# Kernel optimization log

Hardware: AMD Instinct MI355X
Metric: run time of the kernel (lower is better)

The kernel has to match this reference:

```python
import jax, jax.numpy as jnp
import numpy as np

B, N_NOISY, N_CLEAN = 4, 4096, 4500
N_TRAIN = 128          # num_train_points
FRAME_KNN = 32         # K
NUM_CLEAN_NBS = 4      # C
DSM_SIGMA = 0.01
FEAT_KNN = 16          # knn inside feature extractor
FE_HID, FEAT_DIM = 64, 128
HID = 128              # score_net_hidden_dim
NUM_BLOCKS = 4
C_DIM = FEAT_DIM + 3   # z_dim + xyz dim


def _sqdist(a, b):
    # a: (..., n, d), b: (..., m, d) -> (..., n, m)
    return (jnp.sum(a * a, -1)[..., :, None]
            + jnp.sum(b * b, -1)[..., None, :]
            - 2.0 * jnp.einsum('...nd,...md->...nm', a, b))


def _knn_idx(q, ref, k):
    _, idx = jax.lax.top_k(-_sqdist(q, ref), k)
    return idx


def _feature_net(pcl, W1, b1, W2, b2):
    # EdgeConv-style point feature extractor: knn gather -> MLP -> max-reduce
    Bb = pcl.shape[0]
    idx = _knn_idx(pcl, pcl, FEAT_KNN)                       # (B,N,k)
    nbrs = pcl[jnp.arange(Bb)[:, None, None], idx]           # (B,N,k,3)
    ctr = pcl[:, :, None, :]
    edge = jnp.concatenate([jnp.broadcast_to(ctr, nbrs.shape), nbrs - ctr], -1)
    h = jnp.max(jax.nn.relu(edge @ W1 + b1), axis=2)         # (B,N,FE_HID)
    return jax.nn.relu(h @ W2 + b2)                          # (B,N,FEAT_DIM)


def _bn(x, g, b):
    # eval-mode BatchNorm1d with default running stats (mean=0, var=1): affine only
    return x * g + b


def _score_net(x, c, Wp, bp, g0, b0, W0, bf0, g1, b1, W1, bf1, Wc, bc, gO, bO, Wo, bo):
    # x: (M,K,3) centered neighbor frames, c: (M,F) per-point latent -> (M,K,1)
    M, K, _ = x.shape
    c_xyz = jnp.concatenate([x, jnp.broadcast_to(c[:, None, :], (M, K, c.shape[-1]))], -1)
    net = c_xyz @ Wp + bp
    for i in range(NUM_BLOCKS):  # ResnetBlockConv1d, conditioned on c_xyz
        h = jax.nn.relu(_bn(net, g0[i], b0[i])) @ W0[i] + bf0[i]
        dx = jax.nn.relu(_bn(h, g1[i], b1[i])) @ W1[i] + bf1[i]
        net = net + dx + c_xyz @ Wc[i] + bc[i]
    return jax.nn.relu(_bn(net, gO, bO)) @ Wo + bo


def setup_inputs() -> dict:
    key = jax.random.key(0)
    ks = jax.random.split(key, 16)
    s = 0.05
    inp = {
        'pcl_noisy': jax.random.normal(ks[0], (B, N_NOISY, 3), jnp.float32),
        'pcl_clean': jax.random.normal(ks[1], (B, N_CLEAN, 3), jnp.float32),
        'pnt_idx': jax.random.randint(ks[2], (N_TRAIN,), 0, N_NOISY),
        # feature net
        'feW1': s * jax.random.normal(ks[3], (6, FE_HID), jnp.float32),
        'feb1': jnp.zeros((FE_HID,), jnp.float32),
        'feW2': s * jax.random.normal(ks[4], (FE_HID, FEAT_DIM), jnp.float32),
        'feb2': jnp.zeros((FEAT_DIM,), jnp.float32),
        # score net
        'Wp': s * jax.random.normal(ks[5], (C_DIM, HID), jnp.float32),
        'bp': jnp.zeros((HID,), jnp.float32),
        'g0': jnp.ones((NUM_BLOCKS, HID), jnp.float32),
        'b0': jnp.zeros((NUM_BLOCKS, HID), jnp.float32),
        'W0': s * jax.random.normal(ks[6], (NUM_BLOCKS, HID, HID), jnp.float32),
        'bf0': jnp.zeros((NUM_BLOCKS, HID), jnp.float32),
        'g1': jnp.ones((NUM_BLOCKS, HID), jnp.float32),
        'b1': jnp.zeros((NUM_BLOCKS, HID), jnp.float32),
        'W1': s * jax.random.normal(ks[7], (NUM_BLOCKS, HID, HID), jnp.float32),
        'bf1': jnp.zeros((NUM_BLOCKS, HID), jnp.float32),
        'Wc': s * jax.random.normal(ks[8], (NUM_BLOCKS, C_DIM, HID), jnp.float32),
        'bc': jnp.zeros((NUM_BLOCKS, HID), jnp.float32),
        'gO': jnp.ones((HID,), jnp.float32),
        'bO': jnp.zeros((HID,), jnp.float32),
        'Wo': s * jax.random.normal(ks[9], (HID, 1), jnp.float32),
        'bo': jnp.zeros((1,), jnp.float32),
    }
    return inp


def reference(pcl_noisy, pcl_clean, pnt_idx, feW1, feb1, feW2, feb2,
              Wp, bp, g0, b0, W0, bf0, g1, b1, W1, bf1, Wc, bc, gO, bO, Wo, bo):
    Bb, N, _ = pcl_noisy.shape
    n, K, C = pnt_idx.shape[0], FRAME_KNN, NUM_CLEAN_NBS
    bidx = jnp.arange(Bb)[:, None]
    # per-point features at training points
    feat = _feature_net(pcl_noisy, feW1, feb1, feW2, feb2)[:, pnt_idx]  # (B,n,F)
    centers = pcl_noisy[:, pnt_idx]                                     # (B,n,3)
    # xy-KNN over noisy cloud -> gather 3D neighbor frames, center them
    nn_idx = _knn_idx(centers[..., :2], pcl_noisy[..., :2], K)           # (B,n,K)
    frames = pcl_noisy[bidx, nn_idx.reshape(Bb, -1)].reshape(Bb, n, K, 3)
    frames_centered = frames - centers[:, :, None, :]
    # xy-KNN of each frame point into the clean cloud
    cidx = _knn_idx(frames[..., :2].reshape(Bb, n * K, 2), pcl_clean[..., :2], C)
    clean_nbs = pcl_clean[bidx, cidx.reshape(Bb, -1)].reshape(Bb, n, K, C, 3)
    # z-only noise vectors, mean over clean neighbors
    noise_z = jnp.mean(frames[..., 2][..., None] - clean_nbs[..., 2], axis=-1)[..., None]  # (B,n,K,1)
    grad_pred = _score_net(frames_centered.reshape(Bb * n, K, 3), feat.reshape(Bb * n, -1),
                           Wp, bp, g0, b0, W0, bf0, g1, b1, W1, bf1, Wc, bc,
                           gO, bO, Wo, bo).reshape(Bb, n, K, 1)
    grad_target = -noise_z
    loss = 0.5 * jnp.mean(jnp.sum((grad_target - grad_pred) ** 2 * (1.0 / DSM_SIGMA), axis=-1))
    return loss
```

## Files before the change

### kernel.cpp

```cpp
#include <hip/hip_runtime.h>
#include <stdint.h>

#define NB_B 4
#define NN 4096
#define NC 4500
#define NT 128
#define FRAME_K 32
#define FEAT_K 16
#define FE_HID 64
#define FEAT_DIM 128
#define HID 128
#define HIDP (HID + 4)
#define NUM_BLOCKS 4

typedef unsigned long long ull;
typedef __attribute__((ext_vector_type(8))) short bf16x8;
typedef __attribute__((ext_vector_type(4))) float f32x4;

__device__ __forceinline__ ull pack_di(float d, int i) {
    return (((ull)__float_as_uint(d)) << 32) | (uint32_t)(unsigned)i;
}

__device__ __forceinline__ unsigned short f2bf(float f) {
    uint32_t u = __float_as_uint(f);
    return (unsigned short)((u + 0x7fffu + ((u >> 16) & 1u)) >> 16);
}

#define UMIN(a,b) ((a) < (b) ? (a) : (b))

#define INS4(v) do { ull _v=(v); if (_v < t3) { if (_v < t2) { t3=t2; \
    if (_v < t1) { t2=t1; if (_v < t0) { t1=t0; t0=_v; } else t1=_v; } \
    else t2=_v; } else t3=_v; } } while(0)

#define LMIN16(dst, v) do { \
    ull _a0 = UMIN(v[0], v[1]),  _a1 = UMIN(v[2], v[3]); \
    ull _a2 = UMIN(v[4], v[5]),  _a3 = UMIN(v[6], v[7]); \
    ull _a4 = UMIN(v[8], v[9]),  _a5 = UMIN(v[10], v[11]); \
    ull _a6 = UMIN(v[12], v[13]),_a7 = UMIN(v[14], v[15]); \
    ull _b0 = UMIN(_a0, _a1), _b1 = UMIN(_a2, _a3); \
    ull _b2 = UMIN(_a4, _a5), _b3 = UMIN(_a6, _a7); \
    dst = UMIN(UMIN(_b0, _b1), UMIN(_b2, _b3)); \
} while(0)

__global__ __launch_bounds__(256) void k_prep(
    const float* __restrict__ W0, const float* __restrict__ W1,
    unsigned short* __restrict__ W0T, unsigned short* __restrict__ W1T)
{
    int idx = blockIdx.x * 256 + threadIdx.x;
    int k = idx & 127, n = (idx >> 7) & 127, blk = idx >> 14;
    int src = blk * 16384 + k * 128 + n;
    W0T[idx] = f2bf(W0[src]);
    W1T[idx] = f2bf(W1[src]);
}

__global__ __launch_bounds__(256) void k_nbr(
    const float* __restrict__ pcl, const int* __restrict__ pidx,
    const float* __restrict__ W1, const float* __restrict__ b1,
    const float* __restrict__ W2, const float* __restrict__ b2,
    float* __restrict__ feat_out,
    float* __restrict__ frames, float* __restrict__ framesC)
{
    int blk = blockIdx.x;
    int b = blk >> 7;
    int i = blk & 127;
    int t = threadIdx.x;
    int wave = t >> 6, lane = t & 63;
    __shared__ ull wred[2][4];
    __shared__ float nb[FEAT_K][3];
    __shared__ float hmax[FE_HID];
    const float* P = pcl + b * NN * 3;
    int qi = pidx[i];
    float qx = P[qi*3+0], qy = P[qi*3+1], qz = P[qi*3+2];

    ull v3[16], v2[16];
    #pragma unroll
    for (int c2 = 0; c2 < 16; ++c2) {
        int j = t + c2*256;
        float dx = P[j*3+0]-qx, dy = P[j*3+1]-qy, dz = P[j*3+2]-qz;
        float dd2 = dx*dx + dy*dy;
        v2[c2] = pack_di(dd2, j);
        v3[c2] = pack_di(dd2 + dz*dz, j);
    }

    int mysel3 = 0, mysel2 = 0;

    {
        ull mymin;
        LMIN16(mymin, v3);
        for (int r = 0; r < FEAT_K; ++r) {
            ull wm = mymin;
            for (int mask = 1; mask < 64; mask <<= 1) {
                ull o = __shfl_xor(wm, mask, 64);
                wm = UMIN(wm, o);
            }
            if (lane == 0) wred[r & 1][wave] = wm;
            __syncthreads();
            ull w0 = wred[r&1][0], w1 = wred[r&1][1];
            ull w2 = wred[r&1][2], w3 = wred[r&1][3];
            ull ww = UMIN(UMIN(w0, w1), UMIN(w2, w3));
            if (t == r) mysel3 = (int)(ww & 0xffffffffu);
            if (mymin == ww) {
                #pragma unroll
                for (int c2 = 0; c2 < 16; ++c2)
                    if (v3[c2] == ww) v3[c2] = ~0ull;
                LMIN16(mymin, v3);
            }
        }
    }
    {
        ull mymin;
        LMIN16(mymin, v2);
        for (int r = 0; r < FRAME_K; ++r) {
            ull wm = mymin;
            for (int mask = 1; mask < 64; mask <<= 1) {
                ull o = __shfl_xor(wm, mask, 64);
                wm = UMIN(wm, o);
            }
            if (lane == 0) wred[r & 1][wave] = wm;
            __syncthreads();
            ull w0 = wred[r&1][0], w1 = wred[r&1][1];
            ull w2 = wred[r&1][2], w3 = wred[r&1][3];
            ull ww = UMIN(UMIN(w0, w1), UMIN(w2, w3));
            if (t == r) mysel2 = (int)(ww & 0xffffffffu);
            if (mymin == ww) {
                #pragma unroll
                for (int c2 = 0; c2 < 16; ++c2)
                    if (v2[c2] == ww) v2[c2] = ~0ull;
                LMIN16(mymin, v2);
            }
        }
    }

    if (t < FRAME_K) {
        int j = mysel2;
        float fx = P[j*3+0], fy = P[j*3+1], fz = P[j*3+2];
        int o = (blk*FRAME_K + t)*3;
        frames[o+0] = fx; frames[o+1] = fy; frames[o+2] = fz;
        framesC[o+0] = fx-qx; framesC[o+1] = fy-qy; framesC[o+2] = fz-qz;
    }
    if (t < FEAT_K) {
        int j = mysel3;
        nb[t][0] = P[j*3+0]; nb[t][1] = P[j*3+1]; nb[t][2] = P[j*3+2];
    }
    __syncthreads();
    if (t < FE_HID) {
        float base = b1[t] + qx*W1[0*FE_HID+t] + qy*W1[1*FE_HID+t] + qz*W1[2*FE_HID+t];
        float w3 = W1[3*FE_HID+t], w4 = W1[4*FE_HID+t], w5 = W1[5*FE_HID+t];
        float mv = 0.0f;
        #pragma unroll
        for (int j = 0; j < FEAT_K; ++j) {
            float pre = base + (nb[j][0]-qx)*w3 + (nb[j][1]-qy)*w4 + (nb[j][2]-qz)*w5;
            pre = fmaxf(pre, 0.0f);
            mv = fmaxf(mv, pre);
        }
        hmax[t] = mv;
    }
    __syncthreads();
    if (t < FEAT_DIM) {
        float a0 = 0.f, a1 = 0.f, a2 = 0.f, a3 = 0.f;
        #pragma unroll
        for (int u = 0; u < FE_HID; u += 4) {
            a0 += hmax[u+0] * W2[(u+0)*FEAT_DIM + t];
            a1 += hmax[u+1] * W2[(u+1)*FEAT_DIM + t];
            a2 += hmax[u+2] * W2[(u+2)*FEAT_DIM + t];
            a3 += hmax[u+3] * W2[(u+3)*FEAT_DIM + t];
        }
        float acc = b2[t] + (a0 + a1) + (a2 + a3);
        feat_out[blk*FEAT_DIM + t] = fmaxf(acc, 0.0f);
    }
}

__global__ __launch_bounds__(256) void k_clean(
    const float* __restrict__ clean, const float* __restrict__ frames,
    float* __restrict__ gt)
{
    int wave = threadIdx.x >> 6;
    int lane = threadIdx.x & 63;
    int qid = blockIdx.x * 4 + wave;
    int m = qid >> 5;
    int b = m >> 7;
    const float* Cp = clean + b * NC * 3;
    float qx = frames[qid*3+0], qy = frames[qid*3+1], qz = frames[qid*3+2];
    ull t0=~0ull, t1=~0ull, t2=~0ull, t3=~0ull;
    for (int j = lane; j < NC; j += 64) {
        float dx = Cp[j*3+0]-qx, dy = Cp[j*3+1]-qy;
        float d = dx*dx + dy*dy;
        ull v = pack_di(d, j);
        INS4(v);
    }
    for (int mask = 1; mask < 64; mask <<= 1) {
        ull e0 = __shfl_xor(t0, mask, 64);
        ull e1 = __shfl_xor(t1, mask, 64);
        ull e2 = __shfl_xor(t2, mask, 64);
        ull e3 = __shfl_xor(t3, mask, 64);
        INS4(e0); INS4(e1); INS4(e2); INS4(e3);
    }
    if (lane == 0) {
        int i0 = (int)(t0 & 0xffffffffu);
        int i1 = (int)(t1 & 0xffffffffu);
        int i2 = (int)(t2 & 0xffffffffu);
        int i3 = (int)(t3 & 0xffffffffu);
        float mz = 0.25f * (Cp[i0*3+2] + Cp[i1*3+2] + Cp[i2*3+2] + Cp[i3*3+2]);
        gt[qid] = mz - qz;
    }
}

__global__ __launch_bounds__(512, 4) void k_score(
    const float* __restrict__ feat, const float* __restrict__ xc,
    const float* __restrict__ gtv,
    const unsigned short* __restrict__ W0T, const unsigned short* __restrict__ W1T,
    const float* __restrict__ Wp, const float* __restrict__ bp,
    const float* __restrict__ g0, const float* __restrict__ b0,
    const float* __restrict__ bf0,
    const float* __restrict__ g1, const float* __restrict__ b1,
    const float* __restrict__ bf1,
    const float* __restrict__ Wc, const float* __restrict__ bc,
    const float* __restrict__ gO, const float* __restrict__ bO,
    const float* __restrict__ Wo, const float* __restrict__ bo,
    float* __restrict__ loss_part)
{
    int m = blockIdx.x;
    int t = threadIdx.x;
    int c = t & 127, q = t >> 7;
    int w = t >> 6;
    int l = t & 63;
    int l15 = l & 15, lg = l >> 4;
    int col = w * 16 + l15;

    __shared__ float cf[FEAT_DIM];
    __shared__ float xs[FRAME_K][3];
    __shared__ float sh[HID];
    __shared__ float ccs[NUM_BLOCKS][HID];
    __shared__ unsigned short Abuf[FRAME_K * HID];
    __shared__ float actO[FRAME_K][HIDP];
    __shared__ float rsum[FRAME_K];

    if (t < FEAT_DIM) cf[t] = feat[m*FEAT_DIM + t];
    else if (t >= 128 && t < 128 + FRAME_K) {
        int r = t - 128;
        xs[r][0] = xc[(m*FRAME_K+r)*3+0];
        xs[r][1] = xc[(m*FRAME_K+r)*3+1];
        xs[r][2] = xc[(m*FRAME_K+r)*3+2];
    }
    __syncthreads();
    {
        const float* Wcp = Wc + q*(FEAT_DIM+3)*HID;
        float c0 = 0.f, c1 = 0.f, c2 = 0.f, c3 = 0.f;
        #pragma unroll 8
        for (int d = 0; d < FEAT_DIM; d += 4) {
            c0 += cf[d+0] * Wcp[(3+d+0)*HID + c];
            c1 += cf[d+1] * Wcp[(3+d+1)*HID + c];
            c2 += cf[d+2] * Wcp[(3+d+2)*HID + c];
            c3 += cf[d+3] * Wcp[(3+d+3)*HID + c];
        }
        ccs[q][c] = bc[q*HID + c] + (c0 + c1) + (c2 + c3);
    }
    if (q == 0) {
        float a0 = 0.f, a1 = 0.f, a2 = 0.f, a3 = 0.f;
        #pragma unroll 8
        for (int d = 0; d < FEAT_DIM; d += 4) {
            a0 += cf[d+0] * Wp[(3+d+0)*HID + c];
            a1 += cf[d+1] * Wp[(3+d+1)*HID + c];
            a2 += cf[d+2] * Wp[(3+d+2)*HID + c];
            a3 += cf[d+3] * Wp[(3+d+3)*HID + c];
        }
        sh[c] = bp[c] + (a0 + a1) + (a2 + a3);
    }
    __syncthreads();

    float net[2][4];
    {
        float wp0 = Wp[0*HID+col], wp1 = Wp[1*HID+col], wp2 = Wp[2*HID+col];
        float s = sh[col];
        #pragma unroll
        for (int mt = 0; mt < 2; ++mt)
            #pragma unroll
            for (int r = 0; r < 4; ++r) {
                int row = mt*16 + lg*4 + r;
                net[mt][r] = s + xs[row][0]*wp0 + xs[row][1]*wp1 + xs[row][2]*wp2;
            }
    }

    for (int blk = 0; blk < NUM_BLOCKS; ++blk) {
        float g0c = g0[blk*HID+col], b0c = b0[blk*HID+col], bf0c = bf0[blk*HID+col];
        float g1c = g1[blk*HID+col], b1c = b1[blk*HID+col], bf1c = bf1[blk*HID+col];

        #pragma unroll
        for (int mt = 0; mt < 2; ++mt)
            #pragma unroll
            for (int r = 0; r < 4; ++r) {
                int row = mt*16 + lg*4 + r;
                float a = fmaxf(net[mt][r]*g0c + b0c, 0.0f);
                int byte = row*256 + ((col*2) ^ ((row&7)<<4));
                *(unsigned short*)((char*)Abuf + byte) = f2bf(a);
            }
        __syncthreads();

        f32x4 acc[2];
        acc[0] = (f32x4){bf0c, bf0c, bf0c, bf0c};
        acc[1] = (f32x4){bf0c, bf0c, bf0c, bf0c};
        const unsigned short* B0 = W0T + blk*HID*HID + col*HID;
        #pragma unroll
        for (int kt = 0; kt < 4; ++kt) {
            int k0 = kt*32 + lg*8;
            bf16x8 bfrag = *(const bf16x8*)(B0 + k0);
            #pragma unroll
            for (int mt = 0; mt < 2; ++mt) {
                int row = mt*16 + l15;
                int byte = row*256 + ((k0*2) ^ ((row&7)<<4));
                bf16x8 afrag = *(bf16x8*)((char*)Abuf + byte);
                acc[mt] = __builtin_amdgcn_mfma_f32_16x16x32_bf16(afrag, bfrag, acc[mt], 0, 0, 0);
            }
        }
        __syncthreads();

        #pragma unroll
        for (int mt = 0; mt < 2; ++mt)
            #pragma unroll
            for (int r = 0; r < 4; ++r) {
                int row = mt*16 + lg*4 + r;
                float a = fmaxf(acc[mt][r]*g1c + b1c, 0.0f);
                int byte = row*256 + ((col*2) ^ ((row&7)<<4));
                *(unsigned short*)((char*)Abuf + byte) = f2bf(a);
            }
        __syncthreads();

        f32x4 dacc[2];
        dacc[0] = (f32x4){bf1c, bf1c, bf1c, bf1c};
        dacc[1] = (f32x4){bf1c, bf1c, bf1c, bf1c};
        const unsigned short* B1 = W1T + blk*HID*HID + col*HID;
        #pragma unroll
        for (int kt = 0; kt < 4; ++kt) {
            int k0 = kt*32 + lg*8;
            bf16x8 bfrag = *(const bf16x8*)(B1 + k0);
            #pragma unroll
            for (int mt = 0; mt < 2; ++mt) {
                int row = mt*16 + l15;
                int byte = row*256 + ((k0*2) ^ ((row&7)<<4));
                bf16x8 afrag = *(bf16x8*)((char*)Abuf + byte);
                dacc[mt] = __builtin_amdgcn_mfma_f32_16x16x32_bf16(afrag, bfrag, dacc[mt], 0, 0, 0);
            }
        }
        __syncthreads();

        const float* Wcp = Wc + blk*(FEAT_DIM+3)*HID;
        float wc0 = Wcp[0*HID+col], wc1 = Wcp[1*HID+col], wc2 = Wcp[2*HID+col];
        float ccv = ccs[blk][col];
        #pragma unroll
        for (int mt = 0; mt < 2; ++mt)
            #pragma unroll
            for (int r = 0; r < 4; ++r) {
                int row = mt*16 + lg*4 + r;
                net[mt][r] += dacc[mt][r] + xs[row][0]*wc0 + xs[row][1]*wc1
                              + xs[row][2]*wc2 + ccv;
            }
    }

    {
        float gc = gO[col], bcv = bO[col], wo = Wo[col];
        #pragma unroll
        for (int mt = 0; mt < 2; ++mt)
            #pragma unroll
            for (int r = 0; r < 4; ++r) {
                int row = mt*16 + lg*4 + r;
                actO[row][col] = fmaxf(net[mt][r]*gc + bcv, 0.0f) * wo;
            }
    }
    __syncthreads();
    if (t < FRAME_K) {
        float s = 0.0f;
        for (int d = 0; d < HID; d += 4) {
            float4 a4 = *reinterpret_cast<const float4*>(&actO[t][d]);
            s += a4.x + a4.y + a4.z + a4.w;
        }
        float gp = s + bo[0];
        float e = gtv[m*FRAME_K + t] - gp;
        rsum[t] = e*e;
    }
    __syncthreads();
    if (t == 0) {
        float s = 0.0f;
        #pragma unroll
        for (int j = 0; j < FRAME_K; ++j) s += rsum[j];
        loss_part[m] = s;
    }
}

__global__ __launch_bounds__(256) void k_loss(
    const float* __restrict__ lp, float* __restrict__ out)
{
    __shared__ float red[256];
    int t = threadIdx.x;
    red[t] = lp[t] + lp[t+256];
    __syncthreads();
    for (int s = 128; s > 0; s >>= 1) {
        if (t < s) red[t] += red[t+s];
        __syncthreads();
    }
    if (t == 0) out[0] = red[0] * (50.0f / 16384.0f);
}

extern "C" void kernel_launch(void* const* d_in, const int* in_sizes, int n_in,
                              void* d_out, int out_size, void* d_ws, size_t ws_size,
                              hipStream_t stream)
{
    (void)in_sizes; (void)n_in; (void)out_size; (void)ws_size;
    const float* pcl_noisy = (const float*)d_in[0];
    const float* pcl_clean = (const float*)d_in[1];
    const int*   pnt_idx   = (const int*)d_in[2];
    const float* feW1 = (const float*)d_in[3];
    const float* feb1 = (const float*)d_in[4];
    const float* feW2 = (const float*)d_in[5];
    const float* feb2 = (const float*)d_in[6];
    const float* Wp  = (const float*)d_in[7];
    const float* bp  = (const float*)d_in[8];
    const float* g0  = (const float*)d_in[9];
    const float* b0  = (const float*)d_in[10];
    const float* W0  = (const float*)d_in[11];
    const float* bf0 = (const float*)d_in[12];
    const float* g1  = (const float*)d_in[13];
    const float* b1  = (const float*)d_in[14];
    const float* W1  = (const float*)d_in[15];
    const float* bf1 = (const float*)d_in[16];
    const float* Wc  = (const float*)d_in[17];
    const float* bc  = (const float*)d_in[18];
    const float* gO  = (const float*)d_in[19];
    const float* bO  = (const float*)d_in[20];
    const float* Wo  = (const float*)d_in[21];
    const float* bo  = (const float*)d_in[22];

    float* ws = (float*)d_ws;
    float* feat    = ws;
    float* frames  = ws + 65536;
    float* framesC = ws + 65536 + 49152;
    float* gt      = ws + 163840;
    float* lp      = ws + 180224;
    unsigned short* W0T = (unsigned short*)(ws + 180736);
    unsigned short* W1T = (unsigned short*)(ws + 180736 + 32768);

    k_prep  <<<256, 256, 0, stream>>>(W0, W1, W0T, W1T);
    k_nbr   <<<512, 256, 0, stream>>>(pcl_noisy, pnt_idx, feW1, feb1, feW2, feb2,
                                      feat, frames, framesC);
    k_clean <<<4096, 256, 0, stream>>>(pcl_clean, frames, gt);
    k_score <<<512, 512, 0, stream>>>(feat, framesC, gt, W0T, W1T,
                                      Wp, bp, g0, b0, bf0, g1, b1, bf1,
                                      Wc, bc, gO, bO, Wo, bo, lp);
    k_loss  <<<1, 256, 0, stream>>>(lp, (float*)d_out);
}
```

Before: 236.6 us.

## Split clean cloud into SoA and use 8-lane groups with threshold-pruned KNN

The prep kernel now also rewrites the clean cloud into separate xy (float2) and z arrays. k_clean assigns 8 lanes per query instead of a full wave, giving 32 queries per block, and launches 512 blocks instead of 4096. Each lane keeps a running fourth-best threshold and skips the insertion logic when a distance cannot enter its top-4, and the shuffle merge runs over 8 lanes instead of 64. Each lane now scans more points serially, and the threshold branch can diverge within a wave.

Measured after the change: 296.6 us. 1.25x slower.

```diff
diff --git a/kernel.cpp b/kernel.cpp
--- a/kernel.cpp
+++ b/kernel.cpp
@@ -44,13 +44,20 @@
 
 __global__ __launch_bounds__(256) void k_prep(
     const float* __restrict__ W0, const float* __restrict__ W1,
-    unsigned short* __restrict__ W0T, unsigned short* __restrict__ W1T)
+    const float* __restrict__ clean,
+    unsigned short* __restrict__ W0T, unsigned short* __restrict__ W1T,
+    float2* __restrict__ CXY, float* __restrict__ CZ)
 {
     int idx = blockIdx.x * 256 + threadIdx.x;
     int k = idx & 127, n = (idx >> 7) & 127, blk = idx >> 14;
     int src = blk * 16384 + k * 128 + n;
     W0T[idx] = f2bf(W0[src]);
     W1T[idx] = f2bf(W1[src]);
+    if (idx < NB_B * NC) {
+        float x = clean[idx*3+0], y = clean[idx*3+1], z = clean[idx*3+2];
+        CXY[idx] = make_float2(x, y);
+        CZ[idx]  = z;
+    }
 }
 
 __global__ __launch_bounds__(256) void k_nbr(
@@ -171,36 +178,46 @@
 }
 
 __global__ __launch_bounds__(256) void k_clean(
-    const float* __restrict__ clean, const float* __restrict__ frames,
-    float* __restrict__ gt)
-{
-    int wave = threadIdx.x >> 6;
-    int lane = threadIdx.x & 63;
-    int qid = blockIdx.x * 4 + wave;
+    const float2* __restrict__ CXY, const float* __restrict__ CZ,
+    const float* __restrict__ frames, float* __restrict__ gt)
+{
+    int t = threadIdx.x;
+    int wave = t >> 6, lane = t & 63;
+    int g = lane >> 3, sl = lane & 7;
+    int qid = blockIdx.x * 32 + wave * 8 + g;
     int m = qid >> 5;
     int b = m >> 7;
-    const float* Cp = clean + b * NC * 3;
+    const float2* Cxy = CXY + b * NC;
+    const float* Cz  = CZ  + b * NC;
     float qx = frames[qid*3+0], qy = frames[qid*3+1], qz = frames[qid*3+2];
-    ull t0=~0ull, t1=~0ull, t2=~0ull, t3=~0ull;
-    for (int j = lane; j < NC; j += 64) {
-        float dx = Cp[j*3+0]-qx, dy = Cp[j*3+1]-qy;
+
+    const ull SENT = (((ull)0x7F800000u) << 32) | 0xFFFFFFFFu;
+    ull t0=SENT, t1=SENT, t2=SENT, t3=SENT;
+    float th3 = __builtin_inff();
+
+    for (int j = sl; j < NC; j += 8) {
+        float2 p = Cxy[j];
+        float dx = p.x - qx, dy = p.y - qy;
         float d = dx*dx + dy*dy;
-        ull v = pack_di(d, j);
-        INS4(v);
-    }
-    for (int mask = 1; mask < 64; mask <<= 1) {
+        if (d <= th3) {
+            ull v = pack_di(d, j);
+            INS4(v);
+            th3 = __uint_as_float((uint32_t)(t3 >> 32));
+        }
+    }
+    for (int mask = 1; mask < 8; mask <<= 1) {
         ull e0 = __shfl_xor(t0, mask, 64);
         ull e1 = __shfl_xor(t1, mask, 64);
         ull e2 = __shfl_xor(t2, mask, 64);
         ull e3 = __shfl_xor(t3, mask, 64);
         INS4(e0); INS4(e1); INS4(e2); INS4(e3);
     }
-    if (lane == 0) {
+    if (sl == 0) {
         int i0 = (int)(t0 & 0xffffffffu);
         int i1 = (int)(t1 & 0xffffffffu);
         int i2 = (int)(t2 & 0xffffffffu);
         int i3 = (int)(t3 & 0xffffffffu);
-        float mz = 0.25f * (Cp[i0*3+2] + Cp[i1*3+2] + Cp[i2*3+2] + Cp[i3*3+2]);
+        float mz = 0.25f * (Cz[i0] + Cz[i1] + Cz[i2] + Cz[i3]);
         gt[qid] = mz - qz;
     }
 }
@@ -437,11 +454,13 @@
     float* lp      = ws + 180224;
     unsigned short* W0T = (unsigned short*)(ws + 180736);
     unsigned short* W1T = (unsigned short*)(ws + 180736 + 32768);
-
-    k_prep  <<<256, 256, 0, stream>>>(W0, W1, W0T, W1T);
+    float2* CXY = (float2*)(ws + 246272);
+    float*  CZ  = ws + 282272;
+
+    k_prep  <<<256, 256, 0, stream>>>(W0, W1, pcl_clean, W0T, W1T, CXY, CZ);
     k_nbr   <<<512, 256, 0, stream>>>(pcl_noisy, pnt_idx, feW1, feb1, feW2, feb2,
                                       feat, frames, framesC);
-    k_clean <<<4096, 256, 0, stream>>>(pcl_clean, frames, gt);
+    k_clean <<<512, 256, 0, stream>>>(CXY, CZ, frames, gt);
     k_score <<<512, 512, 0, stream>>>(feat, framesC, gt, W0T, W1T,
                                       Wp, bp, g0, b0, bf0, g1, b1, bf1,
                                       Wc, bc, gO, bO, Wo, bo, lp);
```
